# Kernel tuning notes

Hardware: AMD Instinct MI355X
Metric: run time of the kernel (lower is better)

## Reference

```python
import jax, jax.numpy as jnp
import numpy as np

N, E = 50000, 800000          # nodes, edges (avg degree 16)
D_IN, D_H = 128, 128          # input_size, hidden_size


def setup_inputs() -> dict:
    key = jax.random.key(0)
    ks = jax.random.split(key, 10)
    s = 0.05  # param init scale
    return {
        "x": jax.random.normal(ks[0], (N, D_IN), jnp.float32),
        "edge_index": jax.random.randint(ks[1], (2, E), 0, N, jnp.int32),
        "h_prev": jax.random.normal(ks[2], (N, D_H), jnp.float32),
        # reset gate params: xr (Linear with bias), hr (no bias)
        "W_xr": jax.random.normal(ks[3], (D_IN, D_H), jnp.float32) * s,
        "b_xr": jnp.zeros((D_H,), jnp.float32),
        "W_hr": jax.random.normal(ks[4], (D_H, D_H), jnp.float32) * s,
        # update gate params
        "W_xz": jax.random.normal(ks[5], (D_IN, D_H), jnp.float32) * s,
        "b_xz": jnp.zeros((D_H,), jnp.float32),
        "W_hz": jax.random.normal(ks[6], (D_H, D_H), jnp.float32) * s,
        # SAGEConv params: lin_l on mean-aggregated neighbors (bias), lin_r on root (no bias)
        "W_l": jax.random.normal(ks[7], (D_IN + D_H, D_H), jnp.float32) * s,
        "b_l": jnp.zeros((D_H,), jnp.float32),
        "W_r": jax.random.normal(ks[8], (D_IN + D_H, D_H), jnp.float32) * s,
    }


def reference(x, edge_index, h_prev, W_xr, b_xr, W_hr, W_xz, b_xz, W_hz, W_l, b_l, W_r):
    # GRU-style gates
    r = jax.nn.sigmoid(x @ W_xr + b_xr + h_prev @ W_hr)   # [N, D_H]
    z = jax.nn.sigmoid(x @ W_xz + b_xz + h_prev @ W_hz)   # [N, D_H]

    # candidate via single-layer GraphSAGE (SAGEConv, mean aggregation)
    xc = jnp.concatenate([x, r * h_prev], axis=-1)        # [N, D_IN+D_H]
    src, dst = edge_index[0], edge_index[1]
    agg = jax.ops.segment_sum(xc[src], dst, num_segments=N)              # [N, D_IN+D_H]
    cnt = jax.ops.segment_sum(jnp.ones((E,), xc.dtype), dst, num_segments=N)
    mean_nbr = agg / jnp.maximum(cnt, 1.0)[:, None]
    # PyG BasicGNN applies no activation after the last (only) layer, so no tanh here.
    n = mean_nbr @ W_l + b_l + xc @ W_r                   # [N, D_H]

    return (1.0 - z) * n + z * h_prev
```

## Files before the change

### kernel.cpp

```cpp
#include <hip/hip_runtime.h>
#include <hip/hip_bf16.h>

typedef __attribute__((ext_vector_type(8))) short bf16x8;
typedef __attribute__((ext_vector_type(4))) short s16x4;
typedef __attribute__((ext_vector_type(4))) float f32x4;
typedef __attribute__((ext_vector_type(4))) int i32x4;
typedef unsigned short u16;
typedef unsigned int u32;

#define D 128
#define DC 256
#define TILES 8
#define NPART 8
#define CAP 128
#define SWZ(row, dim) (((row) << 7) + ((dim) ^ (((row) & 15) << 3)))

__device__ __forceinline__ float bf2f(u16 b) {
    u32 u = ((u32)b) << 16;
    return __uint_as_float(u);
}
__device__ __forceinline__ u16 f2bf(float f) {
    u32 u = __float_as_uint(f);
    u32 r = (u + 0x7fffu + ((u >> 16) & 1u)) >> 16;
    return (u16)r;
}
__device__ __forceinline__ float sigmoidf_(float x) {
    float e = __builtin_amdgcn_exp2f(-1.4426950408889634f * x);
    return __builtin_amdgcn_rcpf(1.0f + e);
}
__device__ __forceinline__ bf16x8 cvt8(const float* __restrict__ p) {
    f32x4 lo = *(const f32x4*)p;
    f32x4 hi = *(const f32x4*)(p + 4);
    union { bf16x8 v; u16 s[8]; } u;
#pragma unroll
    for (int i = 0; i < 4; i++) {
        u.s[i]     = f2bf(lo[i]);
        u.s[i + 4] = f2bf(hi[i]);
    }
    return u.v;
}

__global__ __launch_bounds__(256) void prepfill_kernel(
    const float* __restrict__ Wxr, const float* __restrict__ Whr,
    const float* __restrict__ Wxz, const float* __restrict__ Whz,
    const float* __restrict__ Wl,  const float* __restrict__ Wr,
    u16* __restrict__ WxrT, u16* __restrict__ WhrT,
    u16* __restrict__ WxzT, u16* __restrict__ WhzT,
    u16* __restrict__ WlT,  u16* __restrict__ WrT,
    const int* __restrict__ ei, int* __restrict__ cnt, int* __restrict__ col2,
    int E, int SL, int PSTEP)
{
    int bid = blockIdx.x;
    int tid = threadIdx.x;
    if (bid < 64) {
        int m = bid >> 4;
        int idx = (bid & 15) * 1024 + tid * 4;
        const float* W = (m == 0) ? Wxr : (m == 1) ? Whr : (m == 2) ? Wxz : Whz;
        u16* Wt        = (m == 0) ? WxrT : (m == 1) ? WhrT : (m == 2) ? WxzT : WhzT;
        f32x4 v = *(const f32x4*)(W + idx);
        int k = idx >> 7, n = idx & 127;
#pragma unroll
        for (int j = 0; j < 4; j++) Wt[(n + j) * D + k] = f2bf(v[j]);
    } else if (bid < 128) {
        int m = (bid - 64) >> 5;
        int idx = ((bid - 64) & 31) * 1024 + tid * 4;
        const float* W = (m == 0) ? Wl : Wr;
        u16* Wt        = (m == 0) ? WlT : WrT;
        f32x4 v = *(const f32x4*)(W + idx);
        int k = idx >> 7, n = idx & 127;
#pragma unroll
        for (int j = 0; j < 4; j++) Wt[(n + j) * DC + k] = f2bf(v[j]);
    } else {
        int k = bid - 128;
        int part = k & (NPART - 1);
        int sidx = k >> 3;
        int lo = part * PSTEP, hi = lo + PSTEP;
        long long base = (long long)sidx * SL;
        long long end  = base + SL; if (end > E) end = E;
        for (long long e = base + tid * 4; e < end; e += 1024) {
            if (e + 4 <= end) {
                i32x4 s4 = *(const i32x4*)(ei + e);
                i32x4 d4 = *(const i32x4*)(ei + (size_t)E + e);
#pragma unroll
                for (int j = 0; j < 4; j++) {
                    int dd = d4[j];
                    if (dd >= lo && dd < hi) {
                        int pos = atomicAdd(&cnt[dd], 1);
                        if (pos < CAP) col2[(size_t)dd * CAP + pos] = s4[j];
                    }
                }
            } else {
                for (long long q = e; q < end; q++) {
                    int dd = ei[(size_t)E + q];
                    if (dd >= lo && dd < hi) {
                        int pos = atomicAdd(&cnt[dd], 1);
                        if (pos < CAP) col2[(size_t)dd * CAP + pos] = ei[q];
                    }
                }
            }
        }
    }
}

__global__ __launch_bounds__(512, 4) void fused_kernel(
    const float* __restrict__ x, const float* __restrict__ h,
    const u16* __restrict__ WxrT, const u16* __restrict__ WhrT,
    const u16* __restrict__ WxzT, const u16* __restrict__ WhzT,
    const u16* __restrict__ WlT,  const u16* __restrict__ WrT,
    const float* __restrict__ bxr, const float* __restrict__ bxz,
    u16* __restrict__ zo, u16* __restrict__ yo, u16* __restrict__ wo, int N)
{
    __shared__ u16 xT[TILES][16 * 128];
    __shared__ u16 hT[TILES][16 * 128];
    const int wave = threadIdx.x >> 6;
    const int lane = threadIdx.x & 63;
    const int quad = lane >> 4;
    const int l15  = lane & 15;
    const int node0 = blockIdx.x * (TILES * 16);
    if (node0 >= N) return;

    {
        int tb = node0 + wave * 16;
        u16* Lx = xT[wave];
        u16* Lh = hT[wave];
#pragma unroll
        for (int it = 0; it < 4; it++) {
            int idx = it * 64 + lane;
            int row = idx >> 4, seg = idx & 15;
            int node = tb + row; if (node >= N) node = N - 1;
            *(bf16x8*)&Lx[SWZ(row, seg * 8)] = cvt8(x + (size_t)node * D + seg * 8);
            *(bf16x8*)&Lh[SWZ(row, seg * 8)] = cvt8(h + (size_t)node * D + seg * 8);
        }
    }
    __syncthreads();

    const int dim = wave * 16 + l15;
    u32 rhp0[TILES], rhp1[TILES];

    {
        const u16* wrx = WxrT + (size_t)dim * D + quad * 8;
        const u16* wrh = WhrT + (size_t)dim * D + quad * 8;
        const u16* wzx = WxzT + (size_t)dim * D + quad * 8;
        const u16* wzh = WhzT + (size_t)dim * D + quad * 8;
        bf16x8 b0[4], b1[4], b2[4], b3[4];
#pragma unroll
        for (int c = 0; c < 4; c++) {
            b0[c] = *(const bf16x8*)(wrx + c * 32);
            b1[c] = *(const bf16x8*)(wrh + c * 32);
            b2[c] = *(const bf16x8*)(wzx + c * 32);
            b3[c] = *(const bf16x8*)(wzh + c * 32);
        }
        float br = bxr[dim];
        float bz = bxz[dim];
#pragma unroll
        for (int t = 0; t < TILES; t++) {
            const u16* Lx = xT[t];
            const u16* Lh = hT[t];
            int tb = node0 + t * 16;
            bf16x8 ax[4], ah[4];
#pragma unroll
            for (int c = 0; c < 4; c++) {
                ax[c] = *(const bf16x8*)&Lx[SWZ(l15, c * 32 + quad * 8)];
                ah[c] = *(const bf16x8*)&Lh[SWZ(l15, c * 32 + quad * 8)];
            }
            f32x4 ar = {0.f,0.f,0.f,0.f};
            f32x4 az = {0.f,0.f,0.f,0.f};
#pragma unroll
            for (int c = 0; c < 4; c++) {
                ar = __builtin_amdgcn_mfma_f32_16x16x32_bf16(ax[c], b0[c], ar, 0, 0, 0);
                ar = __builtin_amdgcn_mfma_f32_16x16x32_bf16(ah[c], b1[c], ar, 0, 0, 0);
                az = __builtin_amdgcn_mfma_f32_16x16x32_bf16(ax[c], b2[c], az, 0, 0, 0);
                az = __builtin_amdgcn_mfma_f32_16x16x32_bf16(ah[c], b3[c], az, 0, 0, 0);
            }
            u32 p0 = 0, p1 = 0;
#pragma unroll
            for (int reg = 0; reg < 4; reg++) {
                int row = quad * 4 + reg;
                int node = tb + row;
                float hv = bf2f(Lh[SWZ(row, dim)]);
                float r  = sigmoidf_(ar[reg] + br);
                float zz = sigmoidf_(az[reg] + bz);
                u32 rh = f2bf(r * hv);
                if (reg == 0) p0 = rh;
                else if (reg == 1) p0 |= rh << 16;
                else if (reg == 2) p1 = rh;
                else p1 |= rh << 16;
                if (node < N) zo[(size_t)node * D + dim] = f2bf(zz);
            }
            rhp0[t] = p0;
            rhp1[t] = p1;
        }
    }
    __syncthreads();

#pragma unroll
    for (int t = 0; t < TILES; t++) {
        u16* Lh = hT[t];
        Lh[SWZ(quad * 4 + 0, dim)] = (u16)(rhp0[t]);
        Lh[SWZ(quad * 4 + 1, dim)] = (u16)(rhp0[t] >> 16);
        Lh[SWZ(quad * 4 + 2, dim)] = (u16)(rhp1[t]);
        Lh[SWZ(quad * 4 + 3, dim)] = (u16)(rhp1[t] >> 16);
    }
    __syncthreads();

    {
        const u16* pl = WlT + (size_t)dim * DC + quad * 8;
        const u16* pr = WrT + (size_t)dim * DC + quad * 8;
        bf16x8 l0[4], l1[4], r0[4], r1[4];
#pragma unroll
        for (int c = 0; c < 4; c++) {
            l0[c] = *(const bf16x8*)(pl + c * 32);
            l1[c] = *(const bf16x8*)(pl + 128 + c * 32);
            r0[c] = *(const bf16x8*)(pr + c * 32);
            r1[c] = *(const bf16x8*)(pr + 128 + c * 32);
        }
#pragma unroll
        for (int t = 0; t < TILES; t++) {
            const u16* Lx  = xT[t];
            const u16* Lrh = hT[t];
            int tb = node0 + t * 16;
            bf16x8 ax[4], arh[4];
#pragma unroll
            for (int c = 0; c < 4; c++) {
                ax[c]  = *(const bf16x8*)&Lx[SWZ(l15, c * 32 + quad * 8)];
                arh[c] = *(const bf16x8*)&Lrh[SWZ(l15, c * 32 + quad * 8)];
            }
            f32x4 ay = {0.f,0.f,0.f,0.f};
            f32x4 aw = {0.f,0.f,0.f,0.f};
#pragma unroll
            for (int c = 0; c < 4; c++) {
                ay = __builtin_amdgcn_mfma_f32_16x16x32_bf16(ax[c],  l0[c], ay, 0, 0, 0);
                ay = __builtin_amdgcn_mfma_f32_16x16x32_bf16(arh[c], l1[c], ay, 0, 0, 0);
                aw = __builtin_amdgcn_mfma_f32_16x16x32_bf16(ax[c],  r0[c], aw, 0, 0, 0);
                aw = __builtin_amdgcn_mfma_f32_16x16x32_bf16(arh[c], r1[c], aw, 0, 0, 0);
            }
#pragma unroll
            for (int reg = 0; reg < 4; reg++) {
                int row = quad * 4 + reg;
                int node = tb + row;
                if (node < N) {
                    yo[(size_t)node * D + dim] = f2bf(ay[reg]);
                    wo[(size_t)node * D + dim] = f2bf(aw[reg]);
                }
            }
        }
    }
}

__global__ __launch_bounds__(256) void pull_kernel(
    const int* __restrict__ cnt, const int* __restrict__ col2,
    const u16* __restrict__ y,
    const u16* __restrict__ z, const u16* __restrict__ w,
    const float* __restrict__ h, const float* __restrict__ bl,
    float* __restrict__ out, int N)
{
    const int wave = threadIdx.x >> 6;
    const int lane = threadIdx.x & 63;
    const int node = blockIdx.x * 4 + wave;
    if (node >= N) return;

    const int d    = cnt[node];
    const int dcl  = (d < CAP) ? d : CAP;
    const int base = node * CAP;
    const int g    = lane >> 4;
    const int l15  = lane & 15;

    const int dcap = (dcl < 64) ? dcl : 64;
    int cols = 0;
    if (lane < dcap) cols = col2[base + lane];

    float a[8] = {0.f,0.f,0.f,0.f,0.f,0.f,0.f,0.f};
    for (int i = 0; i < dcap; i += 8) {
        int e0 = i + g, e1 = i + 4 + g;
        int s0 = __shfl(cols, e0 & 63, 64);
        int s1 = __shfl(cols, e1 & 63, 64);
        bool v0 = e0 < dcap, v1 = e1 < dcap;
        bf16x8 A = {}, B = {};
        if (v0) A = *(const bf16x8*)(y + (size_t)s0 * D + l15 * 8);
        if (v1) B = *(const bf16x8*)(y + (size_t)s1 * D + l15 * 8);
        if (v0) {
#pragma unroll
            for (int j = 0; j < 8; j++) a[j] += bf2f((u16)A[j]);
        }
        if (v1) {
#pragma unroll
            for (int j = 0; j < 8; j++) a[j] += bf2f((u16)B[j]);
        }
    }
    for (int i = 64; i < dcl; i += 4) {
        int e = i + g;
        if (e < dcl) {
            int s = col2[base + e];
            bf16x8 v = *(const bf16x8*)(y + (size_t)s * D + l15 * 8);
#pragma unroll
            for (int j = 0; j < 8; j++) a[j] += bf2f((u16)v[j]);
        }
    }
#pragma unroll
    for (int j = 0; j < 8; j++) {
        a[j] += __shfl_xor(a[j], 16, 64);
        a[j] += __shfl_xor(a[j], 32, 64);
    }
    if (lane < 16) {
        float inv = 1.0f / (float)(d > 0 ? d : 1);
        size_t o16 = (size_t)node * D + l15 * 8;
        bf16x8 zv = *(const bf16x8*)(z + o16);
        bf16x8 wv = *(const bf16x8*)(w + o16);
        f32x4 h0 = *(const f32x4*)(h + o16);
        f32x4 h1 = *(const f32x4*)(h + o16 + 4);
        f32x4 b0 = *(const f32x4*)(bl + l15 * 8);
        f32x4 b1 = *(const f32x4*)(bl + l15 * 8 + 4);
        f32x4 o0, o1;
#pragma unroll
        for (int j = 0; j < 4; j++) {
            float zz = bf2f((u16)zv[j]);
            float nv = a[j] * inv + b0[j] + bf2f((u16)wv[j]);
            o0[j] = (1.0f - zz) * nv + zz * h0[j];
        }
#pragma unroll
        for (int j = 0; j < 4; j++) {
            float zz = bf2f((u16)zv[j + 4]);
            float nv = a[j + 4] * inv + b1[j] + bf2f((u16)wv[j + 4]);
            o1[j] = (1.0f - zz) * nv + zz * h1[j];
        }
        *(f32x4*)(out + o16)     = o0;
        *(f32x4*)(out + o16 + 4) = o1;
    }
}

extern "C" void kernel_launch(void* const* d_in, const int* in_sizes, int n_in,
                              void* d_out, int out_size, void* d_ws, size_t ws_size,
                              hipStream_t stream)
{
    const float* x   = (const float*)d_in[0];
    const int*   ei  = (const int*)d_in[1];
    const float* h   = (const float*)d_in[2];
    const float* Wxr = (const float*)d_in[3];
    const float* bxr = (const float*)d_in[4];
    const float* Whr = (const float*)d_in[5];
    const float* Wxz = (const float*)d_in[6];
    const float* bxz = (const float*)d_in[7];
    const float* Whz = (const float*)d_in[8];
    const float* Wl  = (const float*)d_in[9];
    const float* bl  = (const float*)d_in[10];
    const float* Wr  = (const float*)d_in[11];
    float* out = (float*)d_out;

    const int N = in_sizes[0] / D;
    const int E = in_sizes[1] / 2;
    if (N <= 0 || E <= 0) return;

    char* ws = (char*)d_ws;
    size_t off = 0;
    auto alloc = [&](size_t bytes) -> void* {
        void* p = ws + off;
        off += (bytes + 255) & ~(size_t)255;
        return p;
    };
    u16*   z     = (u16*)  alloc((size_t)N * D * 2);
    u16*   y     = (u16*)  alloc((size_t)N * D * 2);
    u16*   w     = (u16*)  alloc((size_t)N * D * 2);
    int*   cnt   = (int*)  alloc((size_t)N * 4);
    int*   col2  = (int*)  alloc((size_t)N * CAP * 4);
    u16*   WxrT  = (u16*)  alloc((size_t)D * D * 2);
    u16*   WhrT  = (u16*)  alloc((size_t)D * D * 2);
    u16*   WxzT  = (u16*)  alloc((size_t)D * D * 2);
    u16*   WhzT  = (u16*)  alloc((size_t)D * D * 2);
    u16*   WlT   = (u16*)  alloc((size_t)DC * D * 2);
    u16*   WrT   = (u16*)  alloc((size_t)DC * D * 2);
    (void)n_in; (void)out_size;
    if (off > ws_size) return;

    hipMemsetAsync(cnt, 0, (size_t)N * 4, stream);

    const int nsl   = 98;
    const int SL    = (((E + nsl - 1) / nsl) + 3) & ~3;
    const int PSTEP = (N + NPART - 1) / NPART;

    prepfill_kernel<<<128 + NPART * nsl, 256, 0, stream>>>(
        Wxr, Whr, Wxz, Whz, Wl, Wr,
        WxrT, WhrT, WxzT, WhzT, WlT, WrT,
        ei, cnt, col2, E, SL, PSTEP);

    fused_kernel<<<(N + TILES * 16 - 1) / (TILES * 16), 512, 0, stream>>>(
        x, h, WxrT, WhrT, WxzT, WhzT, WlT, WrT, bxr, bxz, z, y, w, N);

    pull_kernel<<<(N + 3) / 4, 256, 0, stream>>>(
        cnt, col2, y, z, w, h, bl, out, N);
}
```

Baseline: 237.1 us.

## Fuse edge bucketing into the GEMM kernel tail and zero counts in prep kernel

Moves the edge scatter that fills the per-destination neighbor lists (atomic counters plus col2 writes) out of the weight-prep kernel and into the end of the fused gate/projection GEMM kernel. Each fused block handles one destination partition of one edge slice after finishing its MFMA work, with slice size derived from the fused grid size. The counter reset moves from a separate hipMemsetAsync into the prep kernel. The goal is to drop a memset launch and overlap the latency-bound atomic scatter with the compute-heavy GEMM blocks. The cost is that fewer, larger slices now run serially after each block's GEMM, which can lengthen the fused kernel's tail.

```diff
diff --git a/kernel.cpp b/kernel.cpp
--- a/kernel.cpp
+++ b/kernel.cpp
@@ -40,15 +40,14 @@
     return u.v;
 }
 
-__global__ __launch_bounds__(256) void prepfill_kernel(
+__global__ __launch_bounds__(256) void prep_kernel(
     const float* __restrict__ Wxr, const float* __restrict__ Whr,
     const float* __restrict__ Wxz, const float* __restrict__ Whz,
     const float* __restrict__ Wl,  const float* __restrict__ Wr,
     u16* __restrict__ WxrT, u16* __restrict__ WhrT,
     u16* __restrict__ WxzT, u16* __restrict__ WhzT,
     u16* __restrict__ WlT,  u16* __restrict__ WrT,
-    const int* __restrict__ ei, int* __restrict__ cnt, int* __restrict__ col2,
-    int E, int SL, int PSTEP)
+    int* __restrict__ cnt, int N)
 {
     int bid = blockIdx.x;
     int tid = threadIdx.x;
@@ -71,13 +70,166 @@
 #pragma unroll
         for (int j = 0; j < 4; j++) Wt[(n + j) * DC + k] = f2bf(v[j]);
     } else {
-        int k = bid - 128;
-        int part = k & (NPART - 1);
-        int sidx = k >> 3;
-        int lo = part * PSTEP, hi = lo + PSTEP;
+        long long g = ((long long)(bid - 128) * 256 + tid) * 4;
+        if (g + 3 < N) *(i32x4*)(cnt + g) = (i32x4){0, 0, 0, 0};
+        else for (long long q = g; q < N; q++) cnt[q] = 0;
+    }
+}
+
+__global__ __launch_bounds__(512, 4) void fused_kernel(
+    const float* __restrict__ x, const float* __restrict__ h,
+    const u16* __restrict__ WxrT, const u16* __restrict__ WhrT,
+    const u16* __restrict__ WxzT, const u16* __restrict__ WhzT,
+    const u16* __restrict__ WlT,  const u16* __restrict__ WrT,
+    const float* __restrict__ bxr, const float* __restrict__ bxz,
+    u16* __restrict__ zo, u16* __restrict__ yo, u16* __restrict__ wo,
+    const int* __restrict__ ei, int* __restrict__ cnt, int* __restrict__ col2,
+    int E, int SL, int PSTEP, int N)
+{
+    __shared__ u16 xT[TILES][16 * 128];
+    __shared__ u16 hT[TILES][16 * 128];
+    const int wave = threadIdx.x >> 6;
+    const int lane = threadIdx.x & 63;
+    const int quad = lane >> 4;
+    const int l15  = lane & 15;
+    const int node0 = blockIdx.x * (TILES * 16);
+
+    if (node0 < N) {
+    {
+        int tb = node0 + wave * 16;
+        u16* Lx = xT[wave];
+        u16* Lh = hT[wave];
+#pragma unroll
+        for (int it = 0; it < 4; it++) {
+            int idx = it * 64 + lane;
+            int row = idx >> 4, seg = idx & 15;
+            int node = tb + row; if (node >= N) node = N - 1;
+            *(bf16x8*)&Lx[SWZ(row, seg * 8)] = cvt8(x + (size_t)node * D + seg * 8);
+            *(bf16x8*)&Lh[SWZ(row, seg * 8)] = cvt8(h + (size_t)node * D + seg * 8);
+        }
+    }
+    __syncthreads();
+
+    const int dim = wave * 16 + l15;
+    u32 rhp0[TILES], rhp1[TILES];
+
+    {
+        const u16* wrx = WxrT + (size_t)dim * D + quad * 8;
+        const u16* wrh = WhrT + (size_t)dim * D + quad * 8;
+        const u16* wzx = WxzT + (size_t)dim * D + quad * 8;
+        const u16* wzh = WhzT + (size_t)dim * D + quad * 8;
+        bf16x8 b0[4], b1[4], b2[4], b3[4];
+#pragma unroll
+        for (int c = 0; c < 4; c++) {
+            b0[c] = *(const bf16x8*)(wrx + c * 32);
+            b1[c] = *(const bf16x8*)(wrh + c * 32);
+            b2[c] = *(const bf16x8*)(wzx + c * 32);
+            b3[c] = *(const bf16x8*)(wzh + c * 32);
+        }
+        float br = bxr[dim];
+        float bz = bxz[dim];
+#pragma unroll
+        for (int t = 0; t < TILES; t++) {
+            const u16* Lx = xT[t];
+            const u16* Lh = hT[t];
+            int tb = node0 + t * 16;
+            bf16x8 ax[4], ah[4];
+#pragma unroll
+            for (int c = 0; c < 4; c++) {
+                ax[c] = *(const bf16x8*)&Lx[SWZ(l15, c * 32 + quad * 8)];
+                ah[c] = *(const bf16x8*)&Lh[SWZ(l15, c * 32 + quad * 8)];
+            }
+            f32x4 ar = {0.f,0.f,0.f,0.f};
+            f32x4 az = {0.f,0.f,0.f,0.f};
+#pragma unroll
+            for (int c = 0; c < 4; c++) {
+                ar = __builtin_amdgcn_mfma_f32_16x16x32_bf16(ax[c], b0[c], ar, 0, 0, 0);
+                ar = __builtin_amdgcn_mfma_f32_16x16x32_bf16(ah[c], b1[c], ar, 0, 0, 0);
+                az = __builtin_amdgcn_mfma_f32_16x16x32_bf16(ax[c], b2[c], az, 0, 0, 0);
+                az = __builtin_amdgcn_mfma_f32_16x16x32_bf16(ah[c], b3[c], az, 0, 0, 0);
+            }
+            u32 p0 = 0, p1 = 0;
+#pragma unroll
+            for (int reg = 0; reg < 4; reg++) {
+                int row = quad * 4 + reg;
+                int node = tb + row;
+                float hv = bf2f(Lh[SWZ(row, dim)]);
+                float r  = sigmoidf_(ar[reg] + br);
+                float zz = sigmoidf_(az[reg] + bz);
+                u32 rh = f2bf(r * hv);
+                if (reg == 0) p0 = rh;
+                else if (reg == 1) p0 |= rh << 16;
+                else if (reg == 2) p1 = rh;
+                else p1 |= rh << 16;
+                if (node < N) zo[(size_t)node * D + dim] = f2bf(zz);
+            }
+            rhp0[t] = p0;
+            rhp1[t] = p1;
+        }
+    }
+    __syncthreads();
+
+#pragma unroll
+    for (int t = 0; t < TILES; t++) {
+        u16* Lh = hT[t];
+        Lh[SWZ(quad * 4 + 0, dim)] = (u16)(rhp0[t]);
+        Lh[SWZ(quad * 4 + 1, dim)] = (u16)(rhp0[t] >> 16);
+        Lh[SWZ(quad * 4 + 2, dim)] = (u16)(rhp1[t]);
+        Lh[SWZ(quad * 4 + 3, dim)] = (u16)(rhp1[t] >> 16);
+    }
+    __syncthreads();
+
+    {
+        const u16* pl = WlT + (size_t)dim * DC + quad * 8;
+        const u16* pr = WrT + (size_t)dim * DC + quad * 8;
+        bf16x8 l0[4], l1[4], r0[4], r1[4];
+#pragma unroll
+        for (int c = 0; c < 4; c++) {
+            l0[c] = *(const bf16x8*)(pl + c * 32);
+            l1[c] = *(const bf16x8*)(pl + 128 + c * 32);
+            r0[c] = *(const bf16x8*)(pr + c * 32);
+            r1[c] = *(const bf16x8*)(pr + 128 + c * 32);
+        }
+#pragma unroll
+        for (int t = 0; t < TILES; t++) {
+            const u16* Lx  = xT[t];
+            const u16* Lrh = hT[t];
+            int tb = node0 + t * 16;
+            bf16x8 ax[4], arh[4];
+#pragma unroll
+            for (int c = 0; c < 4; c++) {
+                ax[c]  = *(const bf16x8*)&Lx[SWZ(l15, c * 32 + quad * 8)];
+                arh[c] = *(const bf16x8*)&Lrh[SWZ(l15, c * 32 + quad * 8)];
+            }
+            f32x4 ay = {0.f,0.f,0.f,0.f};
+            f32x4 aw = {0.f,0.f,0.f,0.f};
+#pragma unroll
+            for (int c = 0; c < 4; c++) {
+                ay = __builtin_amdgcn_mfma_f32_16x16x32_bf16(ax[c],  l0[c], ay, 0, 0, 0);
+                ay = __builtin_amdgcn_mfma_f32_16x16x32_bf16(arh[c], l1[c], ay, 0, 0, 0);
+                aw = __builtin_amdgcn_mfma_f32_16x16x32_bf16(ax[c],  r0[c], aw, 0, 0, 0);
+                aw = __builtin_amdgcn_mfma_f32_16x16x32_bf16(arh[c], r1[c], aw, 0, 0, 0);
+            }
+#pragma unroll
+            for (int reg = 0; reg < 4; reg++) {
+                int row = quad * 4 + reg;
+                int node = tb + row;
+                if (node < N) {
+                    yo[(size_t)node * D + dim] = f2bf(ay[reg]);
+                    wo[(size_t)node * D + dim] = f2bf(aw[reg]);
+                }
+            }
+        }
+    }
+    }
+
+    {
+        const int part = blockIdx.x & (NPART - 1);
+        const int sidx = blockIdx.x >> 3;
+        const int lo = part * PSTEP, hi = lo + PSTEP;
         long long base = (long long)sidx * SL;
         long long end  = base + SL; if (end > E) end = E;
-        for (long long e = base + tid * 4; e < end; e += 1024) {
+        for (long long e = base + threadIdx.x * 4; e < end; e += 2048) {
             if (e + 4 <= end) {
                 i32x4 s4 = *(const i32x4*)(ei + e);
                 i32x4 d4 = *(const i32x4*)(ei + (size_t)E + e);
@@ -96,151 +248,6 @@
                         int pos = atomicAdd(&cnt[dd], 1);
                         if (pos < CAP) col2[(size_t)dd * CAP + pos] = ei[q];
                     }
-                }
-            }
-        }
-    }
-}
-
-__global__ __launch_bounds__(512, 4) void fused_kernel(
-    const float* __restrict__ x, const float* __restrict__ h,
-    const u16* __restrict__ WxrT, const u16* __restrict__ WhrT,
-    const u16* __restrict__ WxzT, const u16* __restrict__ WhzT,
-    const u16* __restrict__ WlT,  const u16* __restrict__ WrT,
-    const float* __restrict__ bxr, const float* __restrict__ bxz,
-    u16* __restrict__ zo, u16* __restrict__ yo, u16* __restrict__ wo, int N)
-{
-    __shared__ u16 xT[TILES][16 * 128];
-    __shared__ u16 hT[TILES][16 * 128];
-    const int wave = threadIdx.x >> 6;
-    const int lane = threadIdx.x & 63;
-    const int quad = lane >> 4;
-    const int l15  = lane & 15;
-    const int node0 = blockIdx.x * (TILES * 16);
-    if (node0 >= N) return;
-
-    {
-        int tb = node0 + wave * 16;
-        u16* Lx = xT[wave];
-        u16* Lh = hT[wave];
-#pragma unroll
-        for (int it = 0; it < 4; it++) {
-            int idx = it * 64 + lane;
-            int row = idx >> 4, seg = idx & 15;
-            int node = tb + row; if (node >= N) node = N - 1;
-            *(bf16x8*)&Lx[SWZ(row, seg * 8)] = cvt8(x + (size_t)node * D + seg * 8);
-            *(bf16x8*)&Lh[SWZ(row, seg * 8)] = cvt8(h + (size_t)node * D + seg * 8);
-        }
-    }
-    __syncthreads();
-
-    const int dim = wave * 16 + l15;
-    u32 rhp0[TILES], rhp1[TILES];
-
-    {
-        const u16* wrx = WxrT + (size_t)dim * D + quad * 8;
-        const u16* wrh = WhrT + (size_t)dim * D + quad * 8;
-        const u16* wzx = WxzT + (size_t)dim * D + quad * 8;
-        const u16* wzh = WhzT + (size_t)dim * D + quad * 8;
-        bf16x8 b0[4], b1[4], b2[4], b3[4];
-#pragma unroll
-        for (int c = 0; c < 4; c++) {
-            b0[c] = *(const bf16x8*)(wrx + c * 32);
-            b1[c] = *(const bf16x8*)(wrh + c * 32);
-            b2[c] = *(const bf16x8*)(wzx + c * 32);
-            b3[c] = *(const bf16x8*)(wzh + c * 32);
-        }
-        float br = bxr[dim];
-        float bz = bxz[dim];
-#pragma unroll
-        for (int t = 0; t < TILES; t++) {
-            const u16* Lx = xT[t];
-            const u16* Lh = hT[t];
-            int tb = node0 + t * 16;
-            bf16x8 ax[4], ah[4];
-#pragma unroll
-            for (int c = 0; c < 4; c++) {
-                ax[c] = *(const bf16x8*)&Lx[SWZ(l15, c * 32 + quad * 8)];
-                ah[c] = *(const bf16x8*)&Lh[SWZ(l15, c * 32 + quad * 8)];
-            }
-            f32x4 ar = {0.f,0.f,0.f,0.f};
-            f32x4 az = {0.f,0.f,0.f,0.f};
-#pragma unroll
-            for (int c = 0; c < 4; c++) {
-                ar = __builtin_amdgcn_mfma_f32_16x16x32_bf16(ax[c], b0[c], ar, 0, 0, 0);
-                ar = __builtin_amdgcn_mfma_f32_16x16x32_bf16(ah[c], b1[c], ar, 0, 0, 0);
-                az = __builtin_amdgcn_mfma_f32_16x16x32_bf16(ax[c], b2[c], az, 0, 0, 0);
-                az = __builtin_amdgcn_mfma_f32_16x16x32_bf16(ah[c], b3[c], az, 0, 0, 0);
-            }
-            u32 p0 = 0, p1 = 0;
-#pragma unroll
-            for (int reg = 0; reg < 4; reg++) {
-                int row = quad * 4 + reg;
-                int node = tb + row;
-                float hv = bf2f(Lh[SWZ(row, dim)]);
-                float r  = sigmoidf_(ar[reg] + br);
-                float zz = sigmoidf_(az[reg] + bz);
-                u32 rh = f2bf(r * hv);
-                if (reg == 0) p0 = rh;
-                else if (reg == 1) p0 |= rh << 16;
-                else if (reg == 2) p1 = rh;
-                else p1 |= rh << 16;
-                if (node < N) zo[(size_t)node * D + dim] = f2bf(zz);
-            }
-            rhp0[t] = p0;
-            rhp1[t] = p1;
-        }
-    }
-    __syncthreads();
-
-#pragma unroll
-    for (int t = 0; t < TILES; t++) {
-        u16* Lh = hT[t];
-        Lh[SWZ(quad * 4 + 0, dim)] = (u16)(rhp0[t]);
-        Lh[SWZ(quad * 4 + 1, dim)] = (u16)(rhp0[t] >> 16);
-        Lh[SWZ(quad * 4 + 2, dim)] = (u16)(rhp1[t]);
-        Lh[SWZ(quad * 4 + 3, dim)] = (u16)(rhp1[t] >> 16);
-    }
-    __syncthreads();
-
-    {
-        const u16* pl = WlT + (size_t)dim * DC + quad * 8;
-        const u16* pr = WrT + (size_t)dim * DC + quad * 8;
-        bf16x8 l0[4], l1[4], r0[4], r1[4];
-#pragma unroll
-        for (int c = 0; c < 4; c++) {
-            l0[c] = *(const bf16x8*)(pl + c * 32);
-            l1[c] = *(const bf16x8*)(pl + 128 + c * 32);
-            r0[c] = *(const bf16x8*)(pr + c * 32);
-            r1[c] = *(const bf16x8*)(pr + 128 + c * 32);
-        }
-#pragma unroll
-        for (int t = 0; t < TILES; t++) {
-            const u16* Lx  = xT[t];
-            const u16* Lrh = hT[t];
-            int tb = node0 + t * 16;
-            bf16x8 ax[4], arh[4];
-#pragma unroll
-            for (int c = 0; c < 4; c++) {
-                ax[c]  = *(const bf16x8*)&Lx[SWZ(l15, c * 32 + quad * 8)];
-                arh[c] = *(const bf16x8*)&Lrh[SWZ(l15, c * 32 + quad * 8)];
-            }
-            f32x4 ay = {0.f,0.f,0.f,0.f};
-            f32x4 aw = {0.f,0.f,0.f,0.f};
-#pragma unroll
-            for (int c = 0; c < 4; c++) {
-                ay = __builtin_amdgcn_mfma_f32_16x16x32_bf16(ax[c],  l0[c], ay, 0, 0, 0);
-                ay = __builtin_amdgcn_mfma_f32_16x16x32_bf16(arh[c], l1[c], ay, 0, 0, 0);
-                aw = __builtin_amdgcn_mfma_f32_16x16x32_bf16(ax[c],  r0[c], aw, 0, 0, 0);
-                aw = __builtin_amdgcn_mfma_f32_16x16x32_bf16(arh[c], r1[c], aw, 0, 0, 0);
-            }
-#pragma unroll
-            for (int reg = 0; reg < 4; reg++) {
-                int row = quad * 4 + reg;
-                int node = tb + row;
-                if (node < N) {
-                    yo[(size_t)node * D + dim] = f2bf(ay[reg]);
-                    wo[(size_t)node * D + dim] = f2bf(aw[reg]);
                 }
             }
         }
@@ -371,19 +378,20 @@
     (void)n_in; (void)out_size;
     if (off > ws_size) return;
 
-    hipMemsetAsync(cnt, 0, (size_t)N * 4, stream);
-
-    const int nsl   = 98;
-    const int SL    = (((E + nsl - 1) / nsl) + 3) & ~3;
-    const int PSTEP = (N + NPART - 1) / NPART;
-
-    prepfill_kernel<<<128 + NPART * nsl, 256, 0, stream>>>(
+    const int nz = (N + 1023) / 1024;
+    prep_kernel<<<128 + nz, 256, 0, stream>>>(
         Wxr, Whr, Wxz, Whz, Wl, Wr,
         WxrT, WhrT, WxzT, WhzT, WlT, WrT,
-        ei, cnt, col2, E, SL, PSTEP);
-
-    fused_kernel<<<(N + TILES * 16 - 1) / (TILES * 16), 512, 0, stream>>>(
-        x, h, WxrT, WhrT, WxzT, WhzT, WlT, WrT, bxr, bxz, z, y, w, N);
+        cnt, N);
+
+    const int nfu = (N + TILES * 16 - 1) / (TILES * 16);
+    int nslmin = nfu / NPART; if (nslmin < 1) nslmin = 1;
+    const int SL    = (((E + nslmin - 1) / nslmin) + 3) & ~3;
+    const int PSTEP = (N + NPART - 1) / NPART;
+
+    fused_kernel<<<nfu, 512, 0, stream>>>(
+        x, h, WxrT, WhrT, WxzT, WhzT, WlT, WrT, bxr, bxz, z, y, w,
+        ei, cnt, col2, E, SL, PSTEP, N);
 
     pull_kernel<<<(N + 3) / 4, 256, 0, stream>>>(
         cnt, col2, y, z, w, h, bl, out, N);
```

Result: no change. 232.6 us (-1.9%).
